# Kernel optimization log

Hardware: AMD Instinct MI355X
Metric: run time of the kernel (lower is better)

The kernel has to match this reference:

```python
import jax, jax.numpy as jnp
import numpy as np
import math

B, T, D, H, L = 8, 1024, 128, 8, 2
DH = D // H            # head dim = 16
F = 2 * D              # ffn hidden = 256 (FFN_EXPANSION=2)
SCALE = math.sqrt(DH)  # sqrt of Q last dim per head


def layernorm(x, g, b):
    m = jnp.mean(x, axis=-1, keepdims=True)
    v = jnp.var(x, axis=-1, keepdims=True)
    return (x - m) * jax.lax.rsqrt(v + 1e-5) * g + b


def setup_inputs() -> dict:
    key = jax.random.key(0)
    ks = jax.random.split(key, 16)
    s = 1.0 / math.sqrt(D)
    r = lambda i, shp: jax.random.normal(ks[i], shp, dtype=jnp.float32) * s
    return {
        "x": jax.random.normal(ks[0], (B, T, D), dtype=jnp.float32),
        "y": jax.random.normal(ks[1], (B, T, D), dtype=jnp.float32),
        # shared qkv projections (no bias), per layer
        "Wq": r(2, (L, D, D)), "Wk": r(3, (L, D, D)), "Wv": r(4, (L, D, D)),
        "Wox": r(5, (L, D, D)), "box": jnp.zeros((L, D), jnp.float32),
        "Woy": r(6, (L, D, D)), "boy": jnp.zeros((L, D), jnp.float32),
        "ln1x_g": jnp.ones((L, D), jnp.float32), "ln1x_b": jnp.zeros((L, D), jnp.float32),
        "ln1y_g": jnp.ones((L, D), jnp.float32), "ln1y_b": jnp.zeros((L, D), jnp.float32),
        "ln2x_g": jnp.ones((L, D), jnp.float32), "ln2x_b": jnp.zeros((L, D), jnp.float32),
        "ln2y_g": jnp.ones((L, D), jnp.float32), "ln2y_b": jnp.zeros((L, D), jnp.float32),
        "fx_w1": r(7, (L, D, F)), "fx_b1": jnp.zeros((L, F), jnp.float32),
        "fx_w2": r(8, (L, F, D)), "fx_b2": jnp.zeros((L, D), jnp.float32),
        "fy_w1": r(9, (L, D, F)), "fy_b1": jnp.zeros((L, F), jnp.float32),
        "fy_w2": r(10, (L, F, D)), "fy_b2": jnp.zeros((L, D), jnp.float32),
    }


def _heads(t):
    # (B,T,D) -> (B,T,H,DH)
    return t.reshape(B, T, H, DH)


def _block(x, y, Wq, Wk, Wv, Wox, box, Woy, boy,
           ln1x_g, ln1x_b, ln1y_g, ln1y_b, ln2x_g, ln2x_b, ln2y_g, ln2y_b,
           fx_w1, fx_b1, fx_w2, fx_b2, fy_w1, fy_b1, fy_w2, fy_b2):
    xn = layernorm(x, ln1x_g, ln1x_b)
    yn = layernorm(y, ln1y_g, ln1y_b)
    # x-branch: Q from y, K/V from x ; y-branch: Q from x, K/V from y
    qx = _heads(yn @ Wq); kx = _heads(xn @ Wk); vx = _heads(xn @ Wv)
    qy = _heads(xn @ Wq); ky = _heads(yn @ Wk); vy = _heads(yn @ Wv)
    ax = jnp.einsum('bthd,bshd->bhts', qx, kx)  # (B,H,T,T)
    ay = jnp.einsum('bthd,bshd->bhts', qy, ky)
    # cat over heads + reshape(B,2,H,T,T) + mean(dim=1) == per-head average
    w = jax.nn.softmax((ax + ay) * (0.5 / SCALE), axis=-1)
    o1 = jnp.einsum('bhts,bshd->bthd', w, vx).reshape(B, T, D) @ Wox + box
    o2 = jnp.einsum('bhts,bshd->bthd', w, vy).reshape(B, T, D) @ Woy + boy
    x = x + o1
    y = y + o2
    xn2 = layernorm(x, ln2x_g, ln2x_b)
    yn2 = layernorm(y, ln2y_g, ln2y_b)
    x = x + jax.nn.gelu(xn2 @ fx_w1 + fx_b1, approximate=False) @ fx_w2 + fx_b2
    y = y + jax.nn.gelu(yn2 @ fy_w1 + fy_b1, approximate=False) @ fy_w2 + fy_b2
    return x, y


def reference(x, y, Wq, Wk, Wv, Wox, box, Woy, boy,
              ln1x_g, ln1x_b, ln1y_g, ln1y_b, ln2x_g, ln2x_b, ln2y_g, ln2y_b,
              fx_w1, fx_b1, fx_w2, fx_b2, fy_w1, fy_b1, fy_w2, fy_b2):
    for i in range(L):
        x, y = _block(x, y, Wq[i], Wk[i], Wv[i], Wox[i], box[i], Woy[i], boy[i],
                      ln1x_g[i], ln1x_b[i], ln1y_g[i], ln1y_b[i],
                      ln2x_g[i], ln2x_b[i], ln2y_g[i], ln2y_b[i],
                      fx_w1[i], fx_b1[i], fx_w2[i], fx_b2[i],
                      fy_w1[i], fy_b1[i], fy_w2[i], fy_b2[i])
    return (x, y)
```

## Files before the change

kernel.cpp:

```cpp
#include <hip/hip_runtime.h>
#include <cstddef>

#define BB   8
#define TT   1024
#define DDIM 128
#define HH   8
#define DHH  16
#define FF   256
#define BT   (BB * TT)

typedef unsigned short u16;
typedef __attribute__((ext_vector_type(8))) short short8;
typedef __attribute__((ext_vector_type(4))) float f32x4;

__device__ __forceinline__ u16 bf(float x) {
  unsigned u = __builtin_bit_cast(unsigned, x);
  u += 0x7fffu + ((u >> 16) & 1u);
  return (u16)(u >> 16);
}
__device__ __forceinline__ u16 bft(float x) {
  return (u16)(__builtin_bit_cast(unsigned, x) >> 16);
}
__device__ __forceinline__ float gelu_f(float x) {
  const float t = x * (0.79788456f + 0.03567740814f * x * x);
  return x / (1.0f + __expf(-2.0f * t));
}

struct PrepP { const float* W; u16* Wt; };
struct SetupArgs {
  PrepP prep[18];
  const float* x_in; const float* y_in;
  const float* ln1xg; const float* ln1xb; const float* ln1yg; const float* ln1yb;
  u16* xn; u16* yn;
};

__global__ __launch_bounds__(256) void setup_k(SetupArgs a) {
  __shared__ float tile[64][65];
  const int u = blockIdx.x;
  const int tid = threadIdx.x;
  if (u < 104) {
    int idx, ti, K, N;
    if (u < 40)      { idx = u >> 2;               ti = u & 3;        K = 128; N = 128; }
    else if (u < 72) { idx = 10 + ((u - 40) >> 3); ti = (u - 40) & 7; K = 128; N = 256; }
    else             { idx = 14 + ((u - 72) >> 3); ti = (u - 72) & 7; K = 256; N = 128; }
    const int n0 = (N == 256) ? (ti & 3) * 64 : (ti & 1) * 64;
    const int k0 = (N == 256) ? (ti >> 2) * 64 : (ti >> 1) * 64;
    const PrepP pp = a.prep[idx];
    #pragma unroll
    for (int t = tid; t < 1024; t += 256) {
      const int kk = t >> 4, nn4 = (t & 15) << 2;
      float4 v = *(const float4*)(pp.W + (size_t)(k0 + kk) * N + n0 + nn4);
      tile[nn4 + 0][kk] = v.x; tile[nn4 + 1][kk] = v.y;
      tile[nn4 + 2][kk] = v.z; tile[nn4 + 3][kk] = v.w;
    }
    __syncthreads();
    #pragma unroll
    for (int t = tid; t < 1024; t += 256) {
      const int nn = t >> 4, kk4 = (t & 15) << 2;
      ushort4 o;
      o.x = bf(tile[nn][kk4 + 0]); o.y = bf(tile[nn][kk4 + 1]);
      o.z = bf(tile[nn][kk4 + 2]); o.w = bf(tile[nn][kk4 + 3]);
      *(ushort4*)(pp.Wt + (size_t)(n0 + nn) * K + k0 + kk4) = o;
    }
  } else {
    const int v_ = u - 104;
    const int which = v_ & 1;
    const int row   = (v_ >> 1) * 4 + (tid >> 6);
    const int lane  = tid & 63;
    const float* in = which ? a.y_in : a.x_in;
    const float* g  = which ? a.ln1yg : a.ln1xg;
    const float* b  = which ? a.ln1yb : a.ln1xb;
    u16* out        = which ? a.yn : a.xn;

    float2 v = *(const float2*)(in + (size_t)row * DDIM + lane * 2);
    float s  = v.x + v.y;
    float sq = v.x * v.x + v.y * v.y;
    #pragma unroll
    for (int off = 32; off >= 1; off >>= 1) {
      s  += __shfl_xor(s, off);
      sq += __shfl_xor(sq, off);
    }
    const float mean = s * (1.0f / DDIM);
    const float var  = sq * (1.0f / DDIM) - mean * mean;
    const float r    = rsqrtf(var + 1e-5f);
    float2 gg = *(const float2*)(g + lane * 2);
    float2 bb = *(const float2*)(b + lane * 2);
    ushort2 o;
    o.x = bf((v.x - mean) * r * gg.x + bb.x);
    o.y = bf((v.y - mean) * r * gg.y + bb.y);
    *(ushort2*)(out + (size_t)row * DDIM + lane * 2) = o;
  }
}

struct GemmP { const u16* A; const u16* Wt; u16* outB; u16* outT; };
struct GemmArgs { GemmP p[6]; };

__global__ __launch_bounds__(256) void gemmf_k(GemmArgs a) {
  const GemmP pp = a.p[blockIdx.z];
  const int m0 = blockIdx.y * 32;
  __shared__ __align__(16) u16 As[32][136];
  __shared__ __align__(16) u16 Bs[128][136];
  const int tid  = threadIdx.x;
  const int w    = tid >> 6;
  const int lane = tid & 63;
  const int l15  = lane & 15;
  const int quad = lane >> 4;
  const int wr = w & 1, wc = w >> 1;

  f32x4 acc[4];
  #pragma unroll
  for (int j = 0; j < 4; ++j) acc[j] = {0.f, 0.f, 0.f, 0.f};

  #pragma unroll
  for (int t = tid; t < 512; t += 256) {
    const int r = t >> 4, g8 = (t & 15) << 3;
    *(short8*)&As[r][g8] = *(const short8*)(pp.A + (size_t)(m0 + r) * 128 + g8);
  }
  #pragma unroll
  for (int t = tid; t < 2048; t += 256) {
    const int r = t >> 4, g8 = (t & 15) << 3;
    *(short8*)&Bs[r][g8] = *(const short8*)(pp.Wt + (size_t)r * 128 + g8);
  }
  __syncthreads();
  #pragma unroll
  for (int ks = 0; ks < 4; ++ks) {
    const short8 ar = *(const short8*)&As[wr * 16 + l15][ks * 32 + quad * 8];
    #pragma unroll
    for (int j = 0; j < 4; ++j) {
      const short8 br = *(const short8*)&Bs[wc * 64 + j * 16 + l15][ks * 32 + quad * 8];
      acc[j] = __builtin_amdgcn_mfma_f32_16x16x32_bf16(ar, br, acc[j], 0, 0, 0);
    }
  }

  if (pp.outT) {
    const int m_base = m0 + wr * 16 + quad * 4;
    const int bb_ = m_base >> 10, s = m_base & 1023;
    #pragma unroll
    for (int j = 0; j < 4; ++j) {
      const int n = wc * 64 + j * 16 + l15;
      const int h = n >> 4, c = n & 15;
      ushort4 o;
      o.x = bf(acc[j][0]); o.y = bf(acc[j][1]);
      o.z = bf(acc[j][2]); o.w = bf(acc[j][3]);
      *(ushort4*)(pp.outT + (((size_t)(bb_ * 8 + h) * 16 + c) << 10) + s) = o;
    }
    return;
  }

  #pragma unroll
  for (int j = 0; j < 4; ++j) {
    const int n = wc * 64 + j * 16 + l15;
    #pragma unroll
    for (int reg = 0; reg < 4; ++reg) {
      const int m = m0 + wr * 16 + quad * 4 + reg;
      pp.outB[(size_t)m * 128 + n] = bf(acc[j][reg]);
    }
  }
}

struct WofnP { const u16* A; const u16* WoT; const float* bo; const float* res;
               const float* g2; const float* b2l;
               const u16* W1t; const float* b1;
               const u16* W2t; const float* b2;
               float* outF; u16* outB; const float* gn; const float* bn; };
struct WofnArgs { WofnP p[2]; int ln; };

__global__ __launch_bounds__(256) void wofn_k(WofnArgs a) {
  const WofnP pp = a.p[blockIdx.y];
  const int m0 = blockIdx.x * 32;
  __shared__ __align__(16) u16 As[32][136];
  __shared__ __align__(16) u16 Bs[128][136];
  __shared__ __align__(16) u16 Hs[32][264];
  __shared__ float2 stats[32][2];
  const int tid  = threadIdx.x;
  const int w    = tid >> 6;
  const int lane = tid & 63;
  const int l15  = lane & 15;
  const int quad = lane >> 4;
  const int wr = w & 1, wc = w >> 1;

  #pragma unroll
  for (int t = tid; t < 512; t += 256) {
    const int r = t >> 4, g8 = (t & 15) << 3;
    *(short8*)&As[r][g8] = *(const short8*)(pp.A + (size_t)(m0 + r) * 128 + g8);
  }
  #pragma unroll
  for (int t = tid; t < 2048; t += 256) {
    const int r = t >> 4, g8 = (t & 15) << 3;
    *(short8*)&Bs[r][g8] = *(const short8*)(pp.WoT + (size_t)r * 128 + g8);
  }
  __syncthreads();
  f32x4 acc[4];
  #pragma unroll
  for (int j = 0; j < 4; ++j) acc[j] = {0.f, 0.f, 0.f, 0.f};
  #pragma unroll
  for (int ks = 0; ks < 4; ++ks) {
    const short8 ar = *(const short8*)&As[wr * 16 + l15][ks * 32 + quad * 8];
    #pragma unroll
    for (int j = 0; j < 4; ++j) {
      const short8 br = *(const short8*)&Bs[wc * 64 + j * 16 + l15][ks * 32 + quad * 8];
      acc[j] = __builtin_amdgcn_mfma_f32_16x16x32_bf16(ar, br, acc[j], 0, 0, 0);
    }
  }

  float xv[4][4];
  #pragma unroll
  for (int j = 0; j < 4; ++j) {
    const int n = wc * 64 + j * 16 + l15;
    const float bias_v = pp.bo[n];
    #pragma unroll
    for (int reg = 0; reg < 4; ++reg) {
      const int m = m0 + wr * 16 + quad * 4 + reg;
      xv[j][reg] = acc[j][reg] + bias_v + pp.res[(size_t)m * 128 + n];
    }
  }

  #pragma unroll
  for (int reg = 0; reg < 4; ++reg) {
    float s = 0.f, q = 0.f;
    #pragma unroll
    for (int j = 0; j < 4; ++j) { const float v = xv[j][reg]; s += v; q += v * v; }
    #pragma unroll
    for (int off = 8; off >= 1; off >>= 1) {
      s += __shfl_xor(s, off, 16);
      q += __shfl_xor(q, off, 16);
    }
    if (l15 == 0) stats[wr * 16 + quad * 4 + reg][wc] = make_float2(s, q);
  }
  __syncthreads();
  #pragma unroll
  for (int reg = 0; reg < 4; ++reg) {
    const int mloc = wr * 16 + quad * 4 + reg;
    const float2 s0 = stats[mloc][0], s1 = stats[mloc][1];
    const float mean = (s0.x + s1.x) * (1.0f / 128.f);
    const float var  = (s0.y + s1.y) * (1.0f / 128.f) - mean * mean;
    const float r    = rsqrtf(var + 1e-5f);
    #pragma unroll
    for (int j = 0; j < 4; ++j) {
      const int n = wc * 64 + j * 16 + l15;
      As[mloc][n] = bf((xv[j][reg] - mean) * r * pp.g2[n] + pp.b2l[n]);
    }
  }
  __syncthreads();

  for (int nh = 0; nh < 2; ++nh) {
    #pragma unroll
    for (int t = tid; t < 2048; t += 256) {
      const int r = t >> 4, g8 = (t & 15) << 3;
      *(short8*)&Bs[r][g8] = *(const short8*)(pp.W1t + (size_t)(nh * 128 + r) * 128 + g8);
    }
    __syncthreads();
    f32x4 a1[4];
    #pragma unroll
    for (int j = 0; j < 4; ++j) a1[j] = {0.f, 0.f, 0.f, 0.f};
    #pragma unroll
    for (int ks = 0; ks < 4; ++ks) {
      const short8 ar = *(const short8*)&As[wr * 16 + l15][ks * 32 + quad * 8];
      #pragma unroll
      for (int j = 0; j < 4; ++j) {
        const short8 br = *(const short8*)&Bs[wc * 64 + j * 16 + l15][ks * 32 + quad * 8];
        a1[j] = __builtin_amdgcn_mfma_f32_16x16x32_bf16(ar, br, a1[j], 0, 0, 0);
      }
    }
    #pragma unroll
    for (int j = 0; j < 4; ++j) {
      const int n = wc * 64 + j * 16 + l15;
      const float bias_v = pp.b1[nh * 128 + n];
      #pragma unroll
      for (int reg = 0; reg < 4; ++reg) {
        const int mloc = wr * 16 + quad * 4 + reg;
        Hs[mloc][nh * 128 + n] = bf(gelu_f(a1[j][reg] + bias_v));
      }
    }
    __syncthreads();
  }

  f32x4 a2[4];
  #pragma unroll
  for (int j = 0; j < 4; ++j) a2[j] = {0.f, 0.f, 0.f, 0.f};
  for (int kh = 0; kh < 2; ++kh) {
    #pragma unroll
    for (int t = tid; t < 2048; t += 256) {
      const int r = t >> 4, g8 = (t & 15) << 3;
      *(short8*)&Bs[r][g8] = *(const short8*)(pp.W2t + (size_t)r * 256 + kh * 128 + g8);
    }
    __syncthreads();
    #pragma unroll
    for (int ks = 0; ks < 4; ++ks) {
      const short8 ar = *(const short8*)&Hs[wr * 16 + l15][kh * 128 + ks * 32 + quad * 8];
      #pragma unroll
      for (int j = 0; j < 4; ++j) {
        const short8 br = *(const short8*)&Bs[wc * 64 + j * 16 + l15][ks * 32 + quad * 8];
        a2[j] = __builtin_amdgcn_mfma_f32_16x16x32_bf16(ar, br, a2[j], 0, 0, 0);
      }
    }
    __syncthreads();
  }

  #pragma unroll
  for (int j = 0; j < 4; ++j) {
    const int n = wc * 64 + j * 16 + l15;
    const float bias_v = pp.b2[n];
    #pragma unroll
    for (int reg = 0; reg < 4; ++reg) {
      const int m = m0 + wr * 16 + quad * 4 + reg;
      const float v = a2[j][reg] + bias_v + xv[j][reg];
      xv[j][reg] = v;
      pp.outF[(size_t)m * 128 + n] = v;
    }
  }
  if (!a.ln) return;
  #pragma unroll
  for (int reg = 0; reg < 4; ++reg) {
    float s = 0.f, q = 0.f;
    #pragma unroll
    for (int j = 0; j < 4; ++j) { const float v = xv[j][reg]; s += v; q += v * v; }
    #pragma unroll
    for (int off = 8; off >= 1; off >>= 1) {
      s += __shfl_xor(s, off, 16);
      q += __shfl_xor(q, off, 16);
    }
    if (l15 == 0) stats[wr * 16 + quad * 4 + reg][wc] = make_float2(s, q);
  }
  __syncthreads();
  #pragma unroll
  for (int reg = 0; reg < 4; ++reg) {
    const int mloc = wr * 16 + quad * 4 + reg;
    const float2 s0 = stats[mloc][0], s1 = stats[mloc][1];
    const float mean = (s0.x + s1.x) * (1.0f / 128.f);
    const float var  = (s0.y + s1.y) * (1.0f / 128.f) - mean * mean;
    const float r    = rsqrtf(var + 1e-5f);
    #pragma unroll
    for (int j = 0; j < 4; ++j) {
      const int n = wc * 64 + j * 16 + l15;
      pp.outB[(size_t)(m0 + mloc) * 128 + n] =
          bf((xv[j][reg] - mean) * r * pp.gn[n] + pp.bn[n]);
    }
  }
}

__global__ __launch_bounds__(256) void attn_k(const u16* __restrict__ qx,
                                              const u16* __restrict__ kx,
                                              const u16* __restrict__ qy,
                                              const u16* __restrict__ ky,
                                              const u16* __restrict__ vtx,
                                              const u16* __restrict__ vty,
                                              u16* __restrict__ o1,
                                              u16* __restrict__ o2) {
  const int t0 = blockIdx.x * 64;
  const int bh = blockIdx.y;
  const int b = bh >> 3, h = bh & 7;
  const size_t base = (size_t)b * TT * DDIM + h * DHH;

  __shared__ __align__(16) u16 Ks[2][64][40];
  __shared__ __align__(16) u16 Vt[2][32][72];
  __shared__ __align__(16) u16 Ps[64][72];

  const int tid  = threadIdx.x;
  const int w    = tid >> 6;
  const int lane = tid & 63;
  const int l15  = lane & 15;
  const int quad = lane >> 4;

  const u16* qp = (quad < 2) ? qx : qy;
  const int dq = (quad & 1) * 8;
  const short8 qa = *(const short8*)(qp + base + (size_t)(t0 + w * 16 + l15) * DDIM + dq);

  f32x4 Of0 = {0.f, 0.f, 0.f, 0.f};
  f32x4 Of1 = {0.f, 0.f, 0.f, 0.f};
  float l_i = 0.f;

  const int ks_s = tid >> 2, ks_c = tid & 3;
  const u16* ks_p = (ks_c < 2) ? kx : ky;
  const int ks_d8 = (ks_c & 1) * 8;
  const int ks_col = (ks_c < 2 ? 0 : 16) + ks_d8;

  const int vs_c = tid >> 3;
  const int vs_s8 = (tid & 7) * 8;
  const u16* vs_row = (vs_c < 16) ? (vtx + (((size_t)bh * 16 + vs_c) << 10))
                                  : (vty + (((size_t)bh * 16 + (vs_c - 16)) << 10));

  #define STAGE(kt, buf)                                                          \
    do {                                                                          \
      const int s0_ = (kt) * 64;                                                  \
      *(short8*)&Ks[buf][ks_s][ks_col] =                                          \
          *(const short8*)(ks_p + base + (size_t)(s0_ + ks_s) * DDIM + ks_d8);    \
      *(short8*)&Vt[buf][vs_c][vs_s8] = *(const short8*)(vs_row + s0_ + vs_s8);   \
    } while (0)

  STAGE(0, 0);

  for (int kt = 0; kt < TT / 64; ++kt) {
    const int buf = kt & 1;
    __syncthreads();
    if (kt + 1 < TT / 64) STAGE(kt + 1, buf ^ 1);

    f32x4 Sf[4];
    #pragma unroll
    for (int t = 0; t < 4; ++t) {
      short8 kb = *(const short8*)&Ks[buf][t * 16 + l15][quad * 8];
      f32x4 z = {0.f, 0.f, 0.f, 0.f};
      Sf[t] = __builtin_amdgcn_mfma_f32_16x16x32_bf16(kb, qa, z, 0, 0, 0);
    }

    #pragma unroll
    for (int t = 0; t < 4; ++t) {
      const float p0 = exp2f(Sf[t][0] * 0.18033688011112042f);
      const float p1 = exp2f(Sf[t][1] * 0.18033688011112042f);
      const float p2 = exp2f(Sf[t][2] * 0.18033688011112042f);
      const float p3 = exp2f(Sf[t][3] * 0.18033688011112042f);
      l_i += p0 + p1 + p2 + p3;
      ushort4 pk;
      pk.x = bft(p0); pk.y = bft(p1); pk.z = bft(p2); pk.w = bft(p3);
      *(ushort4*)&Ps[w * 16 + l15][t * 16 + quad * 4] = pk;
    }

    #pragma unroll
    for (int sh = 0; sh < 2; ++sh) {
      short8 pa  = *(const short8*)&Ps[w * 16 + l15][sh * 32 + quad * 8];
      short8 vb0 = *(const short8*)&Vt[buf][l15][sh * 32 + quad * 8];
      short8 vb1 = *(const short8*)&Vt[buf][16 + l15][sh * 32 + quad * 8];
      Of0 = __builtin_amdgcn_mfma_f32_16x16x32_bf16(pa, vb0, Of0, 0, 0, 0);
      Of1 = __builtin_amdgcn_mfma_f32_16x16x32_bf16(pa, vb1, Of1, 0, 0, 0);
    }
  }
  #undef STAGE

  l_i += __shfl_xor(l_i, 16);
  l_i += __shfl_xor(l_i, 32);
  #pragma unroll
  for (int reg = 0; reg < 4; ++reg) {
    const float lq = __shfl(l_i, quad * 4 + reg, 16);
    const float inv = 1.0f / lq;
    const size_t r = base + (size_t)(t0 + w * 16 + quad * 4 + reg) * DDIM + l15;
    o1[r] = bf(Of0[reg] * inv);
    o2[r] = bf(Of1[reg] * inv);
  }
}

extern "C" void kernel_launch(void* const* d_in, const int* in_sizes, int n_in,
                              void* d_out, int out_size, void* d_ws, size_t ws_size,
                              hipStream_t stream) {
  const float* x_in  = (const float*)d_in[0];
  const float* y_in  = (const float*)d_in[1];
  const float* Wq    = (const float*)d_in[2];
  const float* Wk    = (const float*)d_in[3];
  const float* Wv    = (const float*)d_in[4];
  const float* Wox   = (const float*)d_in[5];
  const float* box   = (const float*)d_in[6];
  const float* Woy   = (const float*)d_in[7];
  const float* boy   = (const float*)d_in[8];
  const float* ln1xg = (const float*)d_in[9];
  const float* ln1xb = (const float*)d_in[10];
  const float* ln1yg = (const float*)d_in[11];
  const float* ln1yb = (const float*)d_in[12];
  const float* ln2xg = (const float*)d_in[13];
  const float* ln2xb = (const float*)d_in[14];
  const float* ln2yg = (const float*)d_in[15];
  const float* ln2yb = (const float*)d_in[16];
  const float* fxw1  = (const float*)d_in[17];
  const float* fxb1  = (const float*)d_in[18];
  const float* fxw2  = (const float*)d_in[19];
  const float* fxb2  = (const float*)d_in[20];
  const float* fyw1  = (const float*)d_in[21];
  const float* fyb1  = (const float*)d_in[22];
  const float* fyw2  = (const float*)d_in[23];
  const float* fyb2  = (const float*)d_in[24];

  const size_t S = (size_t)BT * DDIM;
  float* X = (float*)d_out;
  float* Y = X + S;

  char* wsb = (char*)d_ws;
  auto carve = [&](size_t bytes) { char* p = wsb; wsb += (bytes + 255) & ~(size_t)255; return p; };
  u16* xn  = (u16*)carve(S * 2);
  u16* yn  = (u16*)carve(S * 2);
  u16* qx  = (u16*)carve(S * 2);
  u16* kx  = (u16*)carve(S * 2);
  u16* qy  = (u16*)carve(S * 2);
  u16* ky  = (u16*)carve(S * 2);
  u16* vxT = (u16*)carve(S * 2);
  u16* vyT = (u16*)carve(S * 2);
  u16* ob1 = (u16*)carve(S * 2);
  u16* ob2 = (u16*)carve(S * 2);
  u16* WqT[2], *WkT[2], *WvT[2], *WoxT[2], *WoyT[2];
  u16* f1xT[2], *f1yT[2], *f2xT[2], *f2yT[2];
  for (int l = 0; l < 2; ++l) {
    WqT[l]  = (u16*)carve(16384 * 2);
    WkT[l]  = (u16*)carve(16384 * 2);
    WvT[l]  = (u16*)carve(16384 * 2);
    WoxT[l] = (u16*)carve(16384 * 2);
    WoyT[l] = (u16*)carve(16384 * 2);
    f1xT[l] = (u16*)carve(32768 * 2);
    f1yT[l] = (u16*)carve(32768 * 2);
    f2xT[l] = (u16*)carve(32768 * 2);
    f2yT[l] = (u16*)carve(32768 * 2);
  }

  {
    SetupArgs a;
    int pi = 0;
    for (int l = 0; l < 2; ++l) {
      a.prep[pi++] = {Wq  + (size_t)l * 16384, WqT[l]};
      a.prep[pi++] = {Wk  + (size_t)l * 16384, WkT[l]};
      a.prep[pi++] = {Wv  + (size_t)l * 16384, WvT[l]};
      a.prep[pi++] = {Wox + (size_t)l * 16384, WoxT[l]};
      a.prep[pi++] = {Woy + (size_t)l * 16384, WoyT[l]};
    }
    for (int l = 0; l < 2; ++l) {
      a.prep[pi++] = {fxw1 + (size_t)l * 32768, f1xT[l]};
      a.prep[pi++] = {fyw1 + (size_t)l * 32768, f1yT[l]};
    }
    for (int l = 0; l < 2; ++l) {
      a.prep[pi++] = {fxw2 + (size_t)l * 32768, f2xT[l]};
      a.prep[pi++] = {fyw2 + (size_t)l * 32768, f2yT[l]};
    }
    a.x_in = x_in; a.y_in = y_in;
    a.ln1xg = ln1xg; a.ln1xb = ln1xb; a.ln1yg = ln1yg; a.ln1yb = ln1yb;
    a.xn = xn; a.yn = yn;
    setup_k<<<dim3(104 + 4096), 256, 0, stream>>>(a);
  }

  for (int l = 0; l < 2; ++l) {
    const size_t bo  = (size_t)l * DDIM;
    const size_t fbo = (size_t)l * FF;

    {
      GemmArgs a = {};
      a.p[0] = {yn, WqT[l], qx, nullptr};
      a.p[1] = {xn, WkT[l], kx, nullptr};
      a.p[2] = {xn, WvT[l], nullptr, vxT};
      a.p[3] = {xn, WqT[l], qy, nullptr};
      a.p[4] = {yn, WkT[l], ky, nullptr};
      a.p[5] = {yn, WvT[l], nullptr, vyT};
      gemmf_k<<<dim3(1, BT / 32, 6), 256, 0, stream>>>(a);
    }
    attn_k<<<dim3(TT / 64, BB * HH), 256, 0, stream>>>(qx, kx, qy, ky, vxT, vyT, ob1, ob2);
    {
      const float* resx = (l == 0) ? x_in : X;
      const float* resy = (l == 0) ? y_in : Y;
      WofnArgs a = {}; a.ln = (l == 0) ? 1 : 0;
      a.p[0] = {ob1, WoxT[l], box + bo, resx, ln2xg + bo, ln2xb + bo,
                f1xT[l], fxb1 + fbo, f2xT[l], fxb2 + bo,
                X, (l == 0) ? xn : nullptr,
                (l == 0) ? ln1xg + DDIM : nullptr, (l == 0) ? ln1xb + DDIM : nullptr};
      a.p[1] = {ob2, WoyT[l], boy + bo, resy, ln2yg + bo, ln2yb + bo,
                f1yT[l], fyb1 + fbo, f2yT[l], fyb2 + bo,
                Y, (l == 0) ? yn : nullptr,
                (l == 0) ? ln1yg + DDIM : nullptr, (l == 0) ? ln1yb + DDIM : nullptr};
      wofn_k<<<dim3(BT / 32, 2), 256, 0, stream>>>(a);
    }
  }
}
```

Baseline: 226.4 us.

## Fuse layernorm and QKV projections into setup and wofn kernels

Removes the standalone QKV GEMM kernel and the bf16 xn/yn intermediates. LayerNorm1 output now goes straight into shared memory and the Q/K/V projections run in the same block, both in a new lnqkv kernel for layer 0 and in the tail of wofn_k for layer 1. Weight prep becomes its own small kernel with a 3D grid. This saves two launches and the normalized-activation round trips through global memory, but each row block now does three sequential weight loads and GEMMs with extra syncs. The added tail also lengthens the already heavy wofn kernel.

```diff
diff --git a/kernel.cpp b/kernel.cpp
--- a/kernel.cpp
+++ b/kernel.cpp
@@ -26,80 +26,100 @@
   return x / (1.0f + __expf(-2.0f * t));
 }
 
-struct PrepP { const float* W; u16* Wt; };
-struct SetupArgs {
-  PrepP prep[18];
-  const float* x_in; const float* y_in;
-  const float* ln1xg; const float* ln1xb; const float* ln1yg; const float* ln1yb;
-  u16* xn; u16* yn;
-};
-
-__global__ __launch_bounds__(256) void setup_k(SetupArgs a) {
+__device__ __forceinline__ void qkv_tail(
+    const u16* __restrict__ Wq, const u16* __restrict__ Wk, const u16* __restrict__ Wv,
+    u16* __restrict__ q_out, u16* __restrict__ k_out, u16* __restrict__ vT_out,
+    int m0, u16 (*As)[136], u16 (*Bs)[136]) {
+  const int tid = threadIdx.x;
+  const int w = tid >> 6, lane = tid & 63, l15 = lane & 15, quad = lane >> 4;
+  const int wr = w & 1, wc = w >> 1;
+  const u16* Ws[3] = {Wq, Wk, Wv};
+  #pragma unroll
+  for (int wi = 0; wi < 3; ++wi) {
+    #pragma unroll
+    for (int t = tid; t < 2048; t += 256) {
+      const int r = t >> 4, g8 = (t & 15) << 3;
+      *(short8*)&Bs[r][g8] = *(const short8*)(Ws[wi] + (size_t)r * 128 + g8);
+    }
+    __syncthreads();
+    f32x4 acc[4];
+    #pragma unroll
+    for (int j = 0; j < 4; ++j) acc[j] = {0.f, 0.f, 0.f, 0.f};
+    #pragma unroll
+    for (int ks = 0; ks < 4; ++ks) {
+      const short8 ar = *(const short8*)&As[wr * 16 + l15][ks * 32 + quad * 8];
+      #pragma unroll
+      for (int j = 0; j < 4; ++j) {
+        const short8 br = *(const short8*)&Bs[wc * 64 + j * 16 + l15][ks * 32 + quad * 8];
+        acc[j] = __builtin_amdgcn_mfma_f32_16x16x32_bf16(ar, br, acc[j], 0, 0, 0);
+      }
+    }
+    if (wi == 2) {
+      const int m_base = m0 + wr * 16 + quad * 4;
+      const int bb_ = m_base >> 10, s = m_base & 1023;
+      #pragma unroll
+      for (int j = 0; j < 4; ++j) {
+        const int n = wc * 64 + j * 16 + l15;
+        const int h = n >> 4, c = n & 15;
+        ushort4 o;
+        o.x = bf(acc[j][0]); o.y = bf(acc[j][1]);
+        o.z = bf(acc[j][2]); o.w = bf(acc[j][3]);
+        *(ushort4*)(vT_out + (((size_t)(bb_ * 8 + h) * 16 + c) << 10) + s) = o;
+      }
+    } else {
+      u16* out = (wi == 0) ? q_out : k_out;
+      #pragma unroll
+      for (int j = 0; j < 4; ++j) {
+        const int n = wc * 64 + j * 16 + l15;
+        #pragma unroll
+        for (int reg = 0; reg < 4; ++reg) {
+          const int m = m0 + wr * 16 + quad * 4 + reg;
+          out[(size_t)m * 128 + n] = bf(acc[j][reg]);
+        }
+      }
+    }
+    __syncthreads();
+  }
+}
+
+struct PrepP { const float* W; u16* Wt; int K; int N; };
+struct PrepArgs { PrepP p[18]; };
+
+__global__ __launch_bounds__(256) void prep_k(PrepArgs a) {
+  const PrepP pp = a.p[blockIdx.z];
+  const int n0 = blockIdx.x * 64, k0 = blockIdx.y * 64;
+  if (n0 >= pp.N || k0 >= pp.K) return;
   __shared__ float tile[64][65];
-  const int u = blockIdx.x;
   const int tid = threadIdx.x;
-  if (u < 104) {
-    int idx, ti, K, N;
-    if (u < 40)      { idx = u >> 2;               ti = u & 3;        K = 128; N = 128; }
-    else if (u < 72) { idx = 10 + ((u - 40) >> 3); ti = (u - 40) & 7; K = 128; N = 256; }
-    else             { idx = 14 + ((u - 72) >> 3); ti = (u - 72) & 7; K = 256; N = 128; }
-    const int n0 = (N == 256) ? (ti & 3) * 64 : (ti & 1) * 64;
-    const int k0 = (N == 256) ? (ti >> 2) * 64 : (ti >> 1) * 64;
-    const PrepP pp = a.prep[idx];
-    #pragma unroll
-    for (int t = tid; t < 1024; t += 256) {
-      const int kk = t >> 4, nn4 = (t & 15) << 2;
-      float4 v = *(const float4*)(pp.W + (size_t)(k0 + kk) * N + n0 + nn4);
-      tile[nn4 + 0][kk] = v.x; tile[nn4 + 1][kk] = v.y;
-      tile[nn4 + 2][kk] = v.z; tile[nn4 + 3][kk] = v.w;
-    }
-    __syncthreads();
-    #pragma unroll
-    for (int t = tid; t < 1024; t += 256) {
-      const int nn = t >> 4, kk4 = (t & 15) << 2;
-      ushort4 o;
-      o.x = bf(tile[nn][kk4 + 0]); o.y = bf(tile[nn][kk4 + 1]);
-      o.z = bf(tile[nn][kk4 + 2]); o.w = bf(tile[nn][kk4 + 3]);
-      *(ushort4*)(pp.Wt + (size_t)(n0 + nn) * K + k0 + kk4) = o;
-    }
-  } else {
-    const int v_ = u - 104;
-    const int which = v_ & 1;
-    const int row   = (v_ >> 1) * 4 + (tid >> 6);
-    const int lane  = tid & 63;
-    const float* in = which ? a.y_in : a.x_in;
-    const float* g  = which ? a.ln1yg : a.ln1xg;
-    const float* b  = which ? a.ln1yb : a.ln1xb;
-    u16* out        = which ? a.yn : a.xn;
-
-    float2 v = *(const float2*)(in + (size_t)row * DDIM + lane * 2);
-    float s  = v.x + v.y;
-    float sq = v.x * v.x + v.y * v.y;
-    #pragma unroll
-    for (int off = 32; off >= 1; off >>= 1) {
-      s  += __shfl_xor(s, off);
-      sq += __shfl_xor(sq, off);
-    }
-    const float mean = s * (1.0f / DDIM);
-    const float var  = sq * (1.0f / DDIM) - mean * mean;
-    const float r    = rsqrtf(var + 1e-5f);
-    float2 gg = *(const float2*)(g + lane * 2);
-    float2 bb = *(const float2*)(b + lane * 2);
-    ushort2 o;
-    o.x = bf((v.x - mean) * r * gg.x + bb.x);
-    o.y = bf((v.y - mean) * r * gg.y + bb.y);
-    *(ushort2*)(out + (size_t)row * DDIM + lane * 2) = o;
-  }
-}
-
-struct GemmP { const u16* A; const u16* Wt; u16* outB; u16* outT; };
-struct GemmArgs { GemmP p[6]; };
-
-__global__ __launch_bounds__(256) void gemmf_k(GemmArgs a) {
-  const GemmP pp = a.p[blockIdx.z];
-  const int m0 = blockIdx.y * 32;
+  #pragma unroll
+  for (int t = tid; t < 1024; t += 256) {
+    const int kk = t >> 4, nn4 = (t & 15) << 2;
+    float4 v = *(const float4*)(pp.W + (size_t)(k0 + kk) * pp.N + n0 + nn4);
+    tile[nn4 + 0][kk] = v.x; tile[nn4 + 1][kk] = v.y;
+    tile[nn4 + 2][kk] = v.z; tile[nn4 + 3][kk] = v.w;
+  }
+  __syncthreads();
+  #pragma unroll
+  for (int t = tid; t < 1024; t += 256) {
+    const int nn = t >> 4, kk4 = (t & 15) << 2;
+    ushort4 o;
+    o.x = bf(tile[nn][kk4 + 0]); o.y = bf(tile[nn][kk4 + 1]);
+    o.z = bf(tile[nn][kk4 + 2]); o.w = bf(tile[nn][kk4 + 3]);
+    *(ushort4*)(pp.Wt + (size_t)(n0 + nn) * pp.K + k0 + kk4) = o;
+  }
+}
+
+struct LnqkvP { const float* in; const float* g; const float* b;
+                const u16* Wq; const u16* Wk; const u16* Wv;
+                u16* q_out; u16* k_out; u16* vT_out; };
+struct LnqkvArgs { LnqkvP p[2]; };
+
+__global__ __launch_bounds__(256) void lnqkv_k(LnqkvArgs a) {
+  const LnqkvP pp = a.p[blockIdx.y];
+  const int m0 = blockIdx.x * 32;
   __shared__ __align__(16) u16 As[32][136];
   __shared__ __align__(16) u16 Bs[128][136];
+  __shared__ float2 stats[32][2];
   const int tid  = threadIdx.x;
   const int w    = tid >> 6;
   const int lane = tid & 63;
@@ -107,62 +127,53 @@
   const int quad = lane >> 4;
   const int wr = w & 1, wc = w >> 1;
 
-  f32x4 acc[4];
-  #pragma unroll
-  for (int j = 0; j < 4; ++j) acc[j] = {0.f, 0.f, 0.f, 0.f};
-
-  #pragma unroll
-  for (int t = tid; t < 512; t += 256) {
-    const int r = t >> 4, g8 = (t & 15) << 3;
-    *(short8*)&As[r][g8] = *(const short8*)(pp.A + (size_t)(m0 + r) * 128 + g8);
-  }
-  #pragma unroll
-  for (int t = tid; t < 2048; t += 256) {
-    const int r = t >> 4, g8 = (t & 15) << 3;
-    *(short8*)&Bs[r][g8] = *(const short8*)(pp.Wt + (size_t)r * 128 + g8);
+  float xv[4][4];
+  #pragma unroll
+  for (int j = 0; j < 4; ++j) {
+    const int n = wc * 64 + j * 16 + l15;
+    #pragma unroll
+    for (int reg = 0; reg < 4; ++reg) {
+      const int m = m0 + wr * 16 + quad * 4 + reg;
+      xv[j][reg] = pp.in[(size_t)m * 128 + n];
+    }
+  }
+  #pragma unroll
+  for (int reg = 0; reg < 4; ++reg) {
+    float s = 0.f, q = 0.f;
+    #pragma unroll
+    for (int j = 0; j < 4; ++j) { const float v = xv[j][reg]; s += v; q += v * v; }
+    #pragma unroll
+    for (int off = 8; off >= 1; off >>= 1) {
+      s += __shfl_xor(s, off, 16);
+      q += __shfl_xor(q, off, 16);
+    }
+    if (l15 == 0) stats[wr * 16 + quad * 4 + reg][wc] = make_float2(s, q);
   }
   __syncthreads();
   #pragma unroll
-  for (int ks = 0; ks < 4; ++ks) {
-    const short8 ar = *(const short8*)&As[wr * 16 + l15][ks * 32 + quad * 8];
-    #pragma unroll
-    for (int j = 0; j < 4; ++j) {
-      const short8 br = *(const short8*)&Bs[wc * 64 + j * 16 + l15][ks * 32 + quad * 8];
-      acc[j] = __builtin_amdgcn_mfma_f32_16x16x32_bf16(ar, br, acc[j], 0, 0, 0);
-    }
-  }
-
-  if (pp.outT) {
-    const int m_base = m0 + wr * 16 + quad * 4;
-    const int bb_ = m_base >> 10, s = m_base & 1023;
+  for (int reg = 0; reg < 4; ++reg) {
+    const int mloc = wr * 16 + quad * 4 + reg;
+    const float2 s0 = stats[mloc][0], s1 = stats[mloc][1];
+    const float mean = (s0.x + s1.x) * (1.0f / 128.f);
+    const float var  = (s0.y + s1.y) * (1.0f / 128.f) - mean * mean;
+    const float r    = rsqrtf(var + 1e-5f);
     #pragma unroll
     for (int j = 0; j < 4; ++j) {
       const int n = wc * 64 + j * 16 + l15;
-      const int h = n >> 4, c = n & 15;
-      ushort4 o;
-      o.x = bf(acc[j][0]); o.y = bf(acc[j][1]);
-      o.z = bf(acc[j][2]); o.w = bf(acc[j][3]);
-      *(ushort4*)(pp.outT + (((size_t)(bb_ * 8 + h) * 16 + c) << 10) + s) = o;
-    }
-    return;
-  }
-
-  #pragma unroll
-  for (int j = 0; j < 4; ++j) {
-    const int n = wc * 64 + j * 16 + l15;
-    #pragma unroll
-    for (int reg = 0; reg < 4; ++reg) {
-      const int m = m0 + wr * 16 + quad * 4 + reg;
-      pp.outB[(size_t)m * 128 + n] = bf(acc[j][reg]);
-    }
-  }
+      As[mloc][n] = bf((xv[j][reg] - mean) * r * pp.g[n] + pp.b[n]);
+    }
+  }
+  qkv_tail(pp.Wq, pp.Wk, pp.Wv, pp.q_out, pp.k_out, pp.vT_out, m0, As, Bs);
 }
 
 struct WofnP { const u16* A; const u16* WoT; const float* bo; const float* res;
                const float* g2; const float* b2l;
                const u16* W1t; const float* b1;
                const u16* W2t; const float* b2;
-               float* outF; u16* outB; const float* gn; const float* bn; };
+               float* outF;
+               const float* gn; const float* bn;
+               const u16* nWq; const u16* nWk; const u16* nWv;
+               u16* q_out; u16* k_out; u16* vT_out; };
 struct WofnArgs { WofnP p[2]; int ln; };
 
 __global__ __launch_bounds__(256) void wofn_k(WofnArgs a) {
@@ -310,6 +321,7 @@
     }
   }
   if (!a.ln) return;
+
   #pragma unroll
   for (int reg = 0; reg < 4; ++reg) {
     float s = 0.f, q = 0.f;
@@ -333,10 +345,10 @@
     #pragma unroll
     for (int j = 0; j < 4; ++j) {
       const int n = wc * 64 + j * 16 + l15;
-      pp.outB[(size_t)(m0 + mloc) * 128 + n] =
-          bf((xv[j][reg] - mean) * r * pp.gn[n] + pp.bn[n]);
-    }
-  }
+      As[mloc][n] = bf((xv[j][reg] - mean) * r * pp.gn[n] + pp.bn[n]);
+    }
+  }
+  qkv_tail(pp.nWq, pp.nWk, pp.nWv, pp.q_out, pp.k_out, pp.vT_out, m0, As, Bs);
 }
 
 __global__ __launch_bounds__(256) void attn_k(const u16* __restrict__ qx,
@@ -473,8 +485,6 @@
 
   char* wsb = (char*)d_ws;
   auto carve = [&](size_t bytes) { char* p = wsb; wsb += (bytes + 255) & ~(size_t)255; return p; };
-  u16* xn  = (u16*)carve(S * 2);
-  u16* yn  = (u16*)carve(S * 2);
   u16* qx  = (u16*)carve(S * 2);
   u16* kx  = (u16*)carve(S * 2);
   u16* qy  = (u16*)carve(S * 2);
@@ -498,56 +508,53 @@
   }
 
   {
-    SetupArgs a;
-    int pi = 0;
+    PrepArgs a;
+    int idx = 0;
     for (int l = 0; l < 2; ++l) {
-      a.prep[pi++] = {Wq  + (size_t)l * 16384, WqT[l]};
-      a.prep[pi++] = {Wk  + (size_t)l * 16384, WkT[l]};
-      a.prep[pi++] = {Wv  + (size_t)l * 16384, WvT[l]};
-      a.prep[pi++] = {Wox + (size_t)l * 16384, WoxT[l]};
-      a.prep[pi++] = {Woy + (size_t)l * 16384, WoyT[l]};
-    }
-    for (int l = 0; l < 2; ++l) {
-      a.prep[pi++] = {fxw1 + (size_t)l * 32768, f1xT[l]};
-      a.prep[pi++] = {fyw1 + (size_t)l * 32768, f1yT[l]};
-    }
-    for (int l = 0; l < 2; ++l) {
-      a.prep[pi++] = {fxw2 + (size_t)l * 32768, f2xT[l]};
-      a.prep[pi++] = {fyw2 + (size_t)l * 32768, f2yT[l]};
-    }
-    a.x_in = x_in; a.y_in = y_in;
-    a.ln1xg = ln1xg; a.ln1xb = ln1xb; a.ln1yg = ln1yg; a.ln1yb = ln1yb;
-    a.xn = xn; a.yn = yn;
-    setup_k<<<dim3(104 + 4096), 256, 0, stream>>>(a);
+      a.p[idx++] = {Wq  + (size_t)l * 16384, WqT[l],  128, 128};
+      a.p[idx++] = {Wk  + (size_t)l * 16384, WkT[l],  128, 128};
+      a.p[idx++] = {Wv  + (size_t)l * 16384, WvT[l],  128, 128};
+      a.p[idx++] = {Wox + (size_t)l * 16384, WoxT[l], 128, 128};
+      a.p[idx++] = {Woy + (size_t)l * 16384, WoyT[l], 128, 128};
+      a.p[idx++] = {fxw1 + (size_t)l * 32768, f1xT[l], 128, 256};
+      a.p[idx++] = {fyw1 + (size_t)l * 32768, f1yT[l], 128, 256};
+      a.p[idx++] = {fxw2 + (size_t)l * 32768, f2xT[l], 256, 128};
+      a.p[idx++] = {fyw2 + (size_t)l * 32768, f2yT[l], 256, 128};
+    }
+    prep_k<<<dim3(4, 4, 18), 256, 0, stream>>>(a);
+  }
+
+  {
+    LnqkvArgs a;
+    a.p[0] = {x_in, ln1xg, ln1xb, WqT[0], WkT[0], WvT[0], qy, kx, vxT};
+    a.p[1] = {y_in, ln1yg, ln1yb, WqT[0], WkT[0], WvT[0], qx, ky, vyT};
+    lnqkv_k<<<dim3(BT / 32, 2), 256, 0, stream>>>(a);
   }
 
   for (int l = 0; l < 2; ++l) {
     const size_t bo  = (size_t)l * DDIM;
     const size_t fbo = (size_t)l * FF;
 
-    {
-      GemmArgs a = {};
-      a.p[0] = {yn, WqT[l], qx, nullptr};
-      a.p[1] = {xn, WkT[l], kx, nullptr};
-      a.p[2] = {xn, WvT[l], nullptr, vxT};
-      a.p[3] = {xn, WqT[l], qy, nullptr};
-      a.p[4] = {yn, WkT[l], ky, nullptr};
-      a.p[5] = {yn, WvT[l], nullptr, vyT};
-      gemmf_k<<<dim3(1, BT / 32, 6), 256, 0, stream>>>(a);
-    }
     attn_k<<<dim3(TT / 64, BB * HH), 256, 0, stream>>>(qx, kx, qy, ky, vxT, vyT, ob1, ob2);
+
     {
       const float* resx = (l == 0) ? x_in : X;
       const float* resy = (l == 0) ? y_in : Y;
       WofnArgs a = {}; a.ln = (l == 0) ? 1 : 0;
       a.p[0] = {ob1, WoxT[l], box + bo, resx, ln2xg + bo, ln2xb + bo,
-                f1xT[l], fxb1 + fbo, f2xT[l], fxb2 + bo,
-                X, (l == 0) ? xn : nullptr,
-                (l == 0) ? ln1xg + DDIM : nullptr, (l == 0) ? ln1xb + DDIM : nullptr};
+                f1xT[l], fxb1 + fbo, f2xT[l], fxb2 + bo, X,
+                (l == 0) ? ln1xg + DDIM : nullptr, (l == 0) ? ln1xb + DDIM : nullptr,
+                (l == 0) ? WqT[1] : nullptr, (l == 0) ? WkT[1] : nullptr,
+                (l == 0) ? WvT[1] : nullptr,
+                (l == 0) ? qy : nullptr, (l == 0) ? kx : nullptr,
+                (l == 0) ? vxT : nullptr};
       a.p[1] = {ob2, WoyT[l], boy + bo, resy, ln2yg + bo, ln2yb + bo,
-                f1yT[l], fyb1 + fbo, f2yT[l], fyb2 + bo,
-                Y, (l == 0) ? yn : nullptr,
-                (l == 0) ? ln1yg + DDIM : nullptr, (l == 0) ? ln1yb + DDIM : nullptr};
+                f1yT[l], fyb1 + fbo, f2yT[l], fyb2 + bo, Y,
+                (l == 0) ? ln1yg + DDIM : nullptr, (l == 0) ? ln1yb + DDIM : nullptr,
+                (l == 0) ? WqT[1] : nullptr, (l == 0) ? WkT[1] : nullptr,
+                (l == 0) ? WvT[1] : nullptr,
+                (l == 0) ? qx : nullptr, (l == 0) ? ky : nullptr,
+                (l == 0) ? vyT : nullptr};
       wofn_k<<<dim3(BT / 32, 2), 256, 0, stream>>>(a);
     }
   }
```

New measurement: 222.0 us. About the same (-2.0%).
